# Kernel tuning notes

Hardware: AMD Instinct MI355X
Metric: run time of the kernel (lower is better)

## Reference

```python
import jax, jax.numpy as jnp
import numpy as np

DIM = 512
NUM_HEADS = 8
DIM_HEAD = DIM // NUM_HEADS


def _xavier(key, shape):
    fan_in, fan_out = shape[0], shape[1]
    a = (6.0 / (fan_in + fan_out)) ** 0.5
    return jax.random.uniform(key, shape, jnp.float32, -a, a)


def setup_inputs() -> dict:
    key = jax.random.key(0)
    ks = jax.random.split(key, 8)
    B, N, M = 2, 2048, 2048
    x = jax.random.normal(ks[0], (B, N, DIM), jnp.float32)
    source = jax.random.normal(ks[1], (B, M, DIM), jnp.float32)
    source_mask = jax.random.randint(ks[2], (B, M), 0, 2) > 0
    Wq = _xavier(ks[3], (DIM, DIM)); bq = jnp.zeros((DIM,), jnp.float32)
    Wk = _xavier(ks[4], (DIM, DIM)); bk = jnp.zeros((DIM,), jnp.float32)
    Wv = _xavier(ks[5], (DIM, DIM)); bv = jnp.zeros((DIM,), jnp.float32)
    Wm = _xavier(ks[6], (DIM, DIM)); bm = jnp.zeros((DIM,), jnp.float32)
    return {"x": x, "source": source, "source_mask": source_mask,
            "Wq": Wq, "bq": bq, "Wk": Wk, "bk": bk,
            "Wv": Wv, "bv": bv, "Wm": Wm, "bm": bm}


def reference(x, source, source_mask, Wq, bq, Wk, bk, Wv, bv, Wm, bm):
    B, N, D = x.shape
    M = source.shape[-2]
    H, Dh = NUM_HEADS, DIM_HEAD
    # projections (torch Linear: x @ W^T + b)
    q = (x @ Wq.T + bq).reshape(B, N, H, Dh)
    k = (source @ Wk.T + bk).reshape(B, M, H, Dh)
    v = (source @ Wv.T + bv).reshape(B, M, H, Dh)
    scale = 1.0 / (Dh ** 0.5)
    # scores: [B, N, M, H]
    scores = jnp.einsum('bnhd,bmhd->bnmh', q, k) * scale
    scores = jnp.where(source_mask[:, None, :, None], scores, -jnp.inf)
    prob = jax.nn.softmax(scores, axis=-2)  # softmax over m
    agg = jnp.einsum('bnmh,bmhd->bnhd', prob, v).reshape(B, N, D)
    return agg @ Wm.T + bm
```

## Files before the change

### kernel.cpp

```cpp
#include <hip/hip_runtime.h>
#include <hip/hip_bf16.h>

#define DIMF 512
#define NHEAD 8
#define DHEAD 64
#define BATCH 2
#define SEQN 2048
#define SEQM 2048
#define FPS 40
#define QSCALE 0.18033688011112042f

typedef unsigned short u16;
typedef __attribute__((ext_vector_type(8))) short bf16x8;
typedef __attribute__((ext_vector_type(4))) float f32x4;

static __device__ __forceinline__ u16 f2bf(float f) {
    unsigned u = __float_as_uint(f);
    u += 0x7FFF + ((u >> 16) & 1);
    return (u16)(u >> 16);
}
static __device__ __forceinline__ u16 f2bf_fast(float f) {
    return (u16)((__float_as_uint(f) + 0x8000u) >> 16);
}
static __device__ __forceinline__ ushort4 cvt4(float4 v) {
    return make_ushort4(f2bf(v.x), f2bf(v.y), f2bf(v.z), f2bf(v.w));
}
static __device__ __forceinline__ bf16x8 mask8(const int* p) {
    int4 a = *(const int4*)p;
    int4 b = *(const int4*)(p + 4);
    union { u16 u[8]; bf16x8 v; } r;
    r.u[0] = a.x ? 0x3F80 : 0; r.u[1] = a.y ? 0x3F80 : 0;
    r.u[2] = a.z ? 0x3F80 : 0; r.u[3] = a.w ? 0x3F80 : 0;
    r.u[4] = b.x ? 0x3F80 : 0; r.u[5] = b.y ? 0x3F80 : 0;
    r.u[6] = b.z ? 0x3F80 : 0; r.u[7] = b.w ? 0x3F80 : 0;
    return r.v;
}

static __device__ __forceinline__
void load16(const u16* g, u16* l) {
    __builtin_amdgcn_global_load_lds(
        (const __attribute__((address_space(1))) void*)g,
        (__attribute__((address_space(3))) void*)l,
        16, 0, 0);
}

#define ASZ (64 * FPS)
#define BSZ (128 * FPS)

__device__ __forceinline__
void gemm_mfma(const float* __restrict__ Xf, const u16* __restrict__ Xb,
               const float* __restrict__ Wf, const float* __restrict__ bias,
               const int* __restrict__ msk, void* __restrict__ Out, int mode)
{
    __shared__ __align__(16) u16 SH[2 * ASZ + 2 * BSZ];

    const int tid  = threadIdx.x;
    const int wave = tid >> 6;
    const int lane = tid & 63;
    const int l15  = lane & 15;
    const int quad = lane >> 4;
    const int wm = wave & 1, wn = wave >> 1;
    const int r0 = blockIdx.x * 64, c0 = blockIdx.y * 128;

    f32x4 acc[2][4] = {};

    const int wr = tid >> 1, wh = (tid & 1) * 16;
    const int ar = tid >> 3, aseg = tid & 7;
    const int br = tid >> 2, boct = tid & 3;

    float4 rw[4];
    float4 ra0, ra1;
    bf16x8 rab;

    auto loadg = [&](int k0) {
        #pragma unroll
        for (int j = 0; j < 4; ++j)
            rw[j] = *(const float4*)&Wf[(size_t)(c0 + wr) * DIMF + k0 + wh + 4 * j];
        if (Xf) {
            ra0 = *(const float4*)&Xf[(size_t)(r0 + ar) * DIMF + k0 + aseg * 4];
            ra1 = *(const float4*)&Xf[(size_t)(r0 + ar + 32) * DIMF + k0 + aseg * 4];
        } else {
            rab = *(const bf16x8*)&Xb[(size_t)(r0 + br) * DIMF + k0 + boct * 8];
        }
    };
    auto stage = [&](int buf) {
        u16* As = SH + buf * ASZ;
        u16* Bs = SH + 2 * ASZ + buf * BSZ;
        if (Xf) {
            *(ushort4*)&As[ar * FPS + aseg * 4] = cvt4(ra0);
            *(ushort4*)&As[(ar + 32) * FPS + aseg * 4] = cvt4(ra1);
        } else {
            *(bf16x8*)&As[br * FPS + boct * 8] = rab;
        }
        #pragma unroll
        for (int j = 0; j < 4; ++j)
            *(ushort4*)&Bs[wr * FPS + wh + 4 * j] = cvt4(rw[j]);
    };

    loadg(0);
    stage(0);
    loadg(32);
    __syncthreads();

    const int NK = DIMF / 32;
    for (int kt = 0; kt < NK; ++kt) {
        const int cur = kt & 1;
        if (kt + 1 < NK) stage(cur ^ 1);
        if (kt + 2 < NK) loadg((kt + 2) * 32);
        const u16* As = SH + cur * ASZ;
        const u16* Bs = SH + 2 * ASZ + cur * BSZ;

        bf16x8 af[2], bf[4];
        #pragma unroll
        for (int mi = 0; mi < 2; ++mi)
            af[mi] = *(const bf16x8*)&As[(wm * 32 + mi * 16 + l15) * FPS + quad * 8];
        #pragma unroll
        for (int ni = 0; ni < 4; ++ni)
            bf[ni] = *(const bf16x8*)&Bs[(wn * 64 + ni * 16 + l15) * FPS + quad * 8];
        #pragma unroll
        for (int mi = 0; mi < 2; ++mi)
            #pragma unroll
            for (int ni = 0; ni < 4; ++ni)
                acc[mi][ni] = __builtin_amdgcn_mfma_f32_16x16x32_bf16(
                    af[mi], bf[ni], acc[mi][ni], 0, 0, 0);
        __syncthreads();
    }

    float bb[4];
    #pragma unroll
    for (int ni = 0; ni < 4; ++ni)
        bb[ni] = bias[c0 + wn * 64 + ni * 16 + l15];

    if (mode == 2) {
        u16* T = SH;
        const int b = r0 >> 11;
        const int n_base = r0 & (SEQN - 1);
        #pragma unroll
        for (int hh = 0; hh < 2; ++hh) {
            __syncthreads();
            if (wn == hh) {
                #pragma unroll
                for (int mi = 0; mi < 2; ++mi) {
                    const int rl = wm * 32 + mi * 16 + quad * 4;
                    int4 m4 = *(const int4*)&msk[b * SEQM + n_base + rl];
                    float mm[4];
                    mm[0] = m4.x ? 1.f : 0.f; mm[1] = m4.y ? 1.f : 0.f;
                    mm[2] = m4.z ? 1.f : 0.f; mm[3] = m4.w ? 1.f : 0.f;
                    #pragma unroll
                    for (int ni = 0; ni < 4; ++ni)
                        #pragma unroll
                        for (int r = 0; r < 4; ++r)
                            T[(rl + r) * 72 + ni * 16 + l15] =
                                f2bf((acc[mi][ni][r] + bb[ni]) * mm[r]);
                }
            }
            __syncthreads();
            const int d = tid >> 2, ms = (tid & 3) << 4;
            u16 tmp[16];
            #pragma unroll
            for (int j = 0; j < 16; ++j) tmp[j] = T[(ms + j) * 72 + d];
            const int hgl = (c0 >> 6) + hh;
            u16* dst = (u16*)Out + ((size_t)(b * NHEAD + hgl) * DHEAD + d) * SEQM
                       + n_base + ms;
            *(bf16x8*)&dst[0] = *(bf16x8*)&tmp[0];
            *(bf16x8*)&dst[8] = *(bf16x8*)&tmp[8];
        }
        return;
    }

    #pragma unroll
    for (int mi = 0; mi < 2; ++mi) {
        const int Rbase = r0 + wm * 32 + mi * 16 + quad * 4;
        const int b = Rbase >> 11;
        const int nb = Rbase & (SEQN - 1);
        #pragma unroll
        for (int ni = 0; ni < 4; ++ni) {
            const int C = c0 + wn * 64 + ni * 16 + l15;
            const int h = C >> 6, d = C & 63;
            if (mode == 0) {
                u16* ow = (u16*)Out;
                #pragma unroll
                for (int r = 0; r < 4; ++r)
                    ow[(((size_t)(b * NHEAD + h) * SEQN) + nb + r) * DHEAD + d] =
                        f2bf((acc[mi][ni][r] + bb[ni]) * QSCALE);
            } else if (mode == 1) {
                u16* ow = (u16*)Out;
                #pragma unroll
                for (int r = 0; r < 4; ++r)
                    ow[(((size_t)(b * NHEAD + h) * SEQN) + nb + r) * DHEAD + d] =
                        f2bf(acc[mi][ni][r] + bb[ni]);
            } else {
                float* ow = (float*)Out;
                #pragma unroll
                for (int r = 0; r < 4; ++r)
                    ow[(size_t)(Rbase + r) * DIMF + C] = acc[mi][ni][r] + bb[ni];
            }
        }
    }
}

__global__ __launch_bounds__(256, 3)
void qkv_proj(const float* __restrict__ x, const float* __restrict__ src,
              const float* __restrict__ Wq, const float* __restrict__ bq,
              const float* __restrict__ Wk, const float* __restrict__ bk,
              const float* __restrict__ Wv, const float* __restrict__ bv,
              const int* __restrict__ mask,
              u16* __restrict__ qw, u16* __restrict__ kw, u16* __restrict__ vtw)
{
    const int z = blockIdx.z;
    const float* X = (z == 0) ? x : src;
    const float* W = (z == 0) ? Wq : (z == 1) ? Wk : Wv;
    const float* B = (z == 0) ? bq : (z == 1) ? bk : bv;
    void* O = (z == 0) ? (void*)qw : (z == 1) ? (void*)kw : (void*)vtw;
    gemm_mfma(X, nullptr, W, B, mask, O, z);
}

__global__ __launch_bounds__(256, 3)
void out_proj(const u16* __restrict__ aggb, const float* __restrict__ Wm,
              const float* __restrict__ bm, float* __restrict__ out)
{
    gemm_mfma(nullptr, aggb, Wm, bm, nullptr, (void*)out, 3);
}

__global__ __launch_bounds__(256, 4)
void flash_attn_mfma(const u16* __restrict__ q, const u16* __restrict__ k,
                     const u16* __restrict__ vt, const int* __restrict__ mask,
                     u16* __restrict__ agg)
{
    __shared__ __align__(16) u16 KsD[2][4096];
    __shared__ __align__(16) u16 VtsD[2][4096];
    __shared__ u16 Ps[4 * 16 * FPS];
    float* Osum = (float*)&KsD[0][0];
    float* Lsum = (float*)&VtsD[0][0];

    const int tid  = threadIdx.x;
    const int wave = tid >> 6;
    const int lane = tid & 63;
    const int l15  = lane & 15;
    const int quad = lane >> 4;
    const int qg = wave >> 1, mh = wave & 1;

    const int bid  = blockIdx.x;
    const int xcd  = bid & 7, slot = bid >> 3;
    const int pair = (xcd << 1) | (slot & 1);
    const int b = pair >> 3, h = pair & 7;
    const int n0 = (slot >> 1) * 32;

    const size_t hoff = (size_t)(b * NHEAD + h) * (size_t)SEQM * DHEAD;
    const u16* kb = k  + hoff;
    const u16* vb = vt + hoff;
    const int* mg = mask + b * SEQM;

    const int dr   = lane >> 3;
    const int doct = (lane & 7) ^ (dr & 7);
    const int g0 = wave, g1 = 4 + wave;
    const u16* kq0 = kb + (size_t)(g0 * 8 + dr) * DHEAD + doct * 8;
    const u16* kq1 = kb + (size_t)(g1 * 8 + dr) * DHEAD + doct * 8;
    const u16* vq0 = vb + (size_t)(g0 * 8 + dr) * SEQM + doct * 8;
    const u16* vq1 = vb + (size_t)(g1 * 8 + dr) * SEQM + doct * 8;

    bf16x8 qf[2];
    {
        const u16* qp = q + hoff + (size_t)(n0 + qg * 16 + l15) * DHEAD + quad * 8;
        qf[0] = *(const bf16x8*)qp;
        qf[1] = *(const bf16x8*)(qp + 32);
    }

    load16(kq0, &KsD[0][g0 * 512]);
    load16(kq1, &KsD[0][g1 * 512]);
    load16(vq0, &VtsD[0][g0 * 512]);
    load16(vq1, &VtsD[0][g1 * 512]);
    bf16x8 mf_nxt = mask8(&mg[32 * mh + quad * 8]);

    f32x4 O[4] = {};
    f32x4 lacc = {};
    u16* Pw = Ps + wave * (16 * FPS);
    const int xoct = l15 & 7;

    for (int mt = 0; mt < SEQM / 64; ++mt) {
        const int cur = mt & 1;
        __syncthreads();
        bf16x8 mf = mf_nxt;
        if (mt + 1 < SEQM / 64) {
            const int m1 = (mt + 1) * 64;
            const int nb = cur ^ 1;
            load16(kq0 + (size_t)m1 * DHEAD, &KsD[nb][g0 * 512]);
            load16(kq1 + (size_t)m1 * DHEAD, &KsD[nb][g1 * 512]);
            load16(vq0 + m1, &VtsD[nb][g0 * 512]);
            load16(vq1 + m1, &VtsD[nb][g1 * 512]);
            mf_nxt = mask8(&mg[m1 + 32 * mh + quad * 8]);
        }
        const u16* Ks  = KsD[cur];
        const u16* Vts = VtsD[cur];

        f32x4 st[2] = {};
        #pragma unroll
        for (int sub = 0; sub < 2; ++sub) {
            const int mrow = 32 * mh + 16 * sub + l15;
            #pragma unroll
            for (int c = 0; c < 2; ++c) {
                const int oct = (4 * c + quad) ^ xoct;
                bf16x8 af = *(const bf16x8*)&Ks[mrow * 64 + oct * 8];
                st[sub] = __builtin_amdgcn_mfma_f32_16x16x32_bf16(
                    af, qf[c], st[sub], 0, 0, 0);
            }
        }

        #pragma unroll
        for (int sub = 0; sub < 2; ++sub) {
            ushort4 w4 = make_ushort4(
                f2bf_fast(__builtin_amdgcn_exp2f(st[sub][0])),
                f2bf_fast(__builtin_amdgcn_exp2f(st[sub][1])),
                f2bf_fast(__builtin_amdgcn_exp2f(st[sub][2])),
                f2bf_fast(__builtin_amdgcn_exp2f(st[sub][3])));
            *(ushort4*)&Pw[l15 * FPS + 16 * sub + 4 * quad] = w4;
        }

        bf16x8 pf = *(const bf16x8*)&Pw[l15 * FPS + quad * 8];
        lacc = __builtin_amdgcn_mfma_f32_16x16x32_bf16(pf, mf, lacc, 0, 0, 0);
        #pragma unroll
        for (int sd = 0; sd < 4; ++sd) {
            const int oct = (4 * mh + quad) ^ xoct;
            bf16x8 vf = *(const bf16x8*)&Vts[(16 * sd + l15) * 64 + oct * 8];
            O[sd] = __builtin_amdgcn_mfma_f32_16x16x32_bf16(pf, vf, O[sd], 0, 0, 0);
        }
    }

    __syncthreads();
    if (mh == 1) {
        #pragma unroll
        for (int sd = 0; sd < 4; ++sd)
            #pragma unroll
            for (int r = 0; r < 4; ++r)
                Osum[qg * 1024 + (quad * 4 + r) * 64 + 16 * sd + l15] = O[sd][r];
        if (l15 == 0) {
            #pragma unroll
            for (int r = 0; r < 4; ++r) Lsum[qg * 16 + quad * 4 + r] = lacc[r];
        }
    }
    __syncthreads();
    if (mh == 0) {
        #pragma unroll
        for (int r = 0; r < 4; ++r) {
            const float inv = 1.f / (lacc[r] + Lsum[qg * 16 + quad * 4 + r]);
            const int n = n0 + qg * 16 + quad * 4 + r;
            u16* ag = agg + ((size_t)b * SEQN + n) * DIMF + h * DHEAD + l15;
            #pragma unroll
            for (int sd = 0; sd < 4; ++sd)
                ag[16 * sd] = f2bf((O[sd][r] +
                    Osum[qg * 1024 + (quad * 4 + r) * 64 + 16 * sd + l15]) * inv);
        }
    }
}

extern "C" void kernel_launch(void* const* d_in, const int* in_sizes, int n_in,
                              void* d_out, int out_size, void* d_ws, size_t ws_size,
                              hipStream_t stream)
{
    (void)in_sizes; (void)n_in; (void)out_size; (void)ws_size;
    const float* x      = (const float*)d_in[0];
    const float* source = (const float*)d_in[1];
    const int*   mask   = (const int*)  d_in[2];
    const float* Wq = (const float*)d_in[3]; const float* bq = (const float*)d_in[4];
    const float* Wk = (const float*)d_in[5]; const float* bk = (const float*)d_in[6];
    const float* Wv = (const float*)d_in[7]; const float* bv = (const float*)d_in[8];
    const float* Wm = (const float*)d_in[9]; const float* bm = (const float*)d_in[10];
    float* out = (float*)d_out;

    const size_t SZ = (size_t)BATCH * SEQN * DIMF;
    u16* qw   = (u16*)d_ws;
    u16* kw   = qw  + SZ;
    u16* vtw  = kw  + SZ;
    u16* aggb = vtw + SZ;

    dim3 gproj(4096 / 64, 512 / 128, 3);
    qkv_proj<<<gproj, 256, 0, stream>>>(x, source, Wq, bq, Wk, bk, Wv, bv,
                                        mask, qw, kw, vtw);

    flash_attn_mfma<<<1024, 256, 0, stream>>>(qw, kw, vtw, mask, aggb);

    dim3 gout(4096 / 64, 512 / 128);
    out_proj<<<gout, 256, 0, stream>>>(aggb, Wm, bm, out);
}
```

Measured before the change: 158.8 us.

## Double query rows per attention block to reuse K/V tiles across two query groups

Each flash-attention block now handles 64 query rows instead of 32, with every wave computing two 16-row query subtiles that share the same K and V fragments loaded from LDS. This halves the grid to 512 blocks and halves total K/V global and LDS traffic per query. In exchange it uses more registers (occupancy hint lowered to 3), a larger P scratch buffer and a larger Osum reduction region, and gives fewer blocks for the 256 CUs.

```diff
diff --git a/kernel.cpp b/kernel.cpp
--- a/kernel.cpp
+++ b/kernel.cpp
@@ -222,14 +222,14 @@
     gemm_mfma(nullptr, aggb, Wm, bm, nullptr, (void*)out, 3);
 }
 
-__global__ __launch_bounds__(256, 4)
+__global__ __launch_bounds__(256, 3)
 void flash_attn_mfma(const u16* __restrict__ q, const u16* __restrict__ k,
                      const u16* __restrict__ vt, const int* __restrict__ mask,
                      u16* __restrict__ agg)
 {
     __shared__ __align__(16) u16 KsD[2][4096];
     __shared__ __align__(16) u16 VtsD[2][4096];
-    __shared__ u16 Ps[4 * 16 * FPS];
+    __shared__ u16 Ps[4 * 32 * FPS];
     float* Osum = (float*)&KsD[0][0];
     float* Lsum = (float*)&VtsD[0][0];
 
@@ -244,7 +244,7 @@
     const int xcd  = bid & 7, slot = bid >> 3;
     const int pair = (xcd << 1) | (slot & 1);
     const int b = pair >> 3, h = pair & 7;
-    const int n0 = (slot >> 1) * 32;
+    const int n0 = (slot >> 1) * 64;
 
     const size_t hoff = (size_t)(b * NHEAD + h) * (size_t)SEQM * DHEAD;
     const u16* kb = k  + hoff;
@@ -259,11 +259,13 @@
     const u16* vq0 = vb + (size_t)(g0 * 8 + dr) * SEQM + doct * 8;
     const u16* vq1 = vb + (size_t)(g1 * 8 + dr) * SEQM + doct * 8;
 
-    bf16x8 qf[2];
-    {
-        const u16* qp = q + hoff + (size_t)(n0 + qg * 16 + l15) * DHEAD + quad * 8;
-        qf[0] = *(const bf16x8*)qp;
-        qf[1] = *(const bf16x8*)(qp + 32);
+    bf16x8 qf[2][2];
+    #pragma unroll
+    for (int qh = 0; qh < 2; ++qh) {
+        const u16* qp = q + hoff + (size_t)(n0 + qg * 32 + qh * 16 + l15) * DHEAD
+                        + quad * 8;
+        qf[qh][0] = *(const bf16x8*)qp;
+        qf[qh][1] = *(const bf16x8*)(qp + 32);
     }
 
     load16(kq0, &KsD[0][g0 * 512]);
@@ -272,9 +274,9 @@
     load16(vq1, &VtsD[0][g1 * 512]);
     bf16x8 mf_nxt = mask8(&mg[32 * mh + quad * 8]);
 
-    f32x4 O[4] = {};
-    f32x4 lacc = {};
-    u16* Pw = Ps + wave * (16 * FPS);
+    f32x4 O[2][4] = {};
+    f32x4 lacc[2] = {};
+    u16* Pw = Ps + wave * (32 * FPS);
     const int xoct = l15 & 7;
 
     for (int mt = 0; mt < SEQM / 64; ++mt) {
@@ -293,7 +295,7 @@
         const u16* Ks  = KsD[cur];
         const u16* Vts = VtsD[cur];
 
-        f32x4 st[2] = {};
+        f32x4 st[2][2] = {};
         #pragma unroll
         for (int sub = 0; sub < 2; ++sub) {
             const int mrow = 32 * mh + 16 * sub + l15;
@@ -301,55 +303,76 @@
             for (int c = 0; c < 2; ++c) {
                 const int oct = (4 * c + quad) ^ xoct;
                 bf16x8 af = *(const bf16x8*)&Ks[mrow * 64 + oct * 8];
-                st[sub] = __builtin_amdgcn_mfma_f32_16x16x32_bf16(
-                    af, qf[c], st[sub], 0, 0, 0);
-            }
-        }
-
-        #pragma unroll
-        for (int sub = 0; sub < 2; ++sub) {
-            ushort4 w4 = make_ushort4(
-                f2bf_fast(__builtin_amdgcn_exp2f(st[sub][0])),
-                f2bf_fast(__builtin_amdgcn_exp2f(st[sub][1])),
-                f2bf_fast(__builtin_amdgcn_exp2f(st[sub][2])),
-                f2bf_fast(__builtin_amdgcn_exp2f(st[sub][3])));
-            *(ushort4*)&Pw[l15 * FPS + 16 * sub + 4 * quad] = w4;
-        }
-
-        bf16x8 pf = *(const bf16x8*)&Pw[l15 * FPS + quad * 8];
-        lacc = __builtin_amdgcn_mfma_f32_16x16x32_bf16(pf, mf, lacc, 0, 0, 0);
+                #pragma unroll
+                for (int qh = 0; qh < 2; ++qh)
+                    st[qh][sub] = __builtin_amdgcn_mfma_f32_16x16x32_bf16(
+                        af, qf[qh][c], st[qh][sub], 0, 0, 0);
+            }
+        }
+
+        #pragma unroll
+        for (int qh = 0; qh < 2; ++qh)
+            #pragma unroll
+            for (int sub = 0; sub < 2; ++sub) {
+                ushort4 w4 = make_ushort4(
+                    f2bf_fast(__builtin_amdgcn_exp2f(st[qh][sub][0])),
+                    f2bf_fast(__builtin_amdgcn_exp2f(st[qh][sub][1])),
+                    f2bf_fast(__builtin_amdgcn_exp2f(st[qh][sub][2])),
+                    f2bf_fast(__builtin_amdgcn_exp2f(st[qh][sub][3])));
+                *(ushort4*)&Pw[(qh * 16 + l15) * FPS + 16 * sub + 4 * quad] = w4;
+            }
+
+        bf16x8 vf[4];
         #pragma unroll
         for (int sd = 0; sd < 4; ++sd) {
             const int oct = (4 * mh + quad) ^ xoct;
-            bf16x8 vf = *(const bf16x8*)&Vts[(16 * sd + l15) * 64 + oct * 8];
-            O[sd] = __builtin_amdgcn_mfma_f32_16x16x32_bf16(pf, vf, O[sd], 0, 0, 0);
+            vf[sd] = *(const bf16x8*)&Vts[(16 * sd + l15) * 64 + oct * 8];
+        }
+
+        #pragma unroll
+        for (int qh = 0; qh < 2; ++qh) {
+            bf16x8 pf = *(const bf16x8*)&Pw[(qh * 16 + l15) * FPS + quad * 8];
+            lacc[qh] = __builtin_amdgcn_mfma_f32_16x16x32_bf16(pf, mf, lacc[qh], 0, 0, 0);
+            #pragma unroll
+            for (int sd = 0; sd < 4; ++sd)
+                O[qh][sd] = __builtin_amdgcn_mfma_f32_16x16x32_bf16(
+                    pf, vf[sd], O[qh][sd], 0, 0, 0);
         }
     }
 
     __syncthreads();
     if (mh == 1) {
         #pragma unroll
-        for (int sd = 0; sd < 4; ++sd)
-            #pragma unroll
-            for (int r = 0; r < 4; ++r)
-                Osum[qg * 1024 + (quad * 4 + r) * 64 + 16 * sd + l15] = O[sd][r];
-        if (l15 == 0) {
-            #pragma unroll
-            for (int r = 0; r < 4; ++r) Lsum[qg * 16 + quad * 4 + r] = lacc[r];
+        for (int qh = 0; qh < 2; ++qh) {
+            #pragma unroll
+            for (int sd = 0; sd < 4; ++sd)
+                #pragma unroll
+                for (int r = 0; r < 4; ++r)
+                    Osum[qg * 2048 + (qh * 16 + quad * 4 + r) * 64 + 16 * sd + l15]
+                        = O[qh][sd][r];
+            if (l15 == 0) {
+                #pragma unroll
+                for (int r = 0; r < 4; ++r)
+                    Lsum[qg * 32 + qh * 16 + quad * 4 + r] = lacc[qh][r];
+            }
         }
     }
     __syncthreads();
     if (mh == 0) {
         #pragma unroll
-        for (int r = 0; r < 4; ++r) {
-            const float inv = 1.f / (lacc[r] + Lsum[qg * 16 + quad * 4 + r]);
-            const int n = n0 + qg * 16 + quad * 4 + r;
-            u16* ag = agg + ((size_t)b * SEQN + n) * DIMF + h * DHEAD + l15;
-            #pragma unroll
-            for (int sd = 0; sd < 4; ++sd)
-                ag[16 * sd] = f2bf((O[sd][r] +
-                    Osum[qg * 1024 + (quad * 4 + r) * 64 + 16 * sd + l15]) * inv);
-        }
+        for (int qh = 0; qh < 2; ++qh)
+            #pragma unroll
+            for (int r = 0; r < 4; ++r) {
+                const float inv = 1.f /
+                    (lacc[qh][r] + Lsum[qg * 32 + qh * 16 + quad * 4 + r]);
+                const int n = n0 + qg * 32 + qh * 16 + quad * 4 + r;
+                u16* ag = agg + ((size_t)b * SEQN + n) * DIMF + h * DHEAD + l15;
+                #pragma unroll
+                for (int sd = 0; sd < 4; ++sd)
+                    ag[16 * sd] = f2bf((O[qh][sd][r] +
+                        Osum[qg * 2048 + (qh * 16 + quad * 4 + r) * 64 + 16 * sd + l15])
+                        * inv);
+            }
     }
 }
 
@@ -377,7 +400,7 @@
     qkv_proj<<<gproj, 256, 0, stream>>>(x, source, Wq, bq, Wk, bk, Wv, bv,
                                         mask, qw, kw, vtw);
 
-    flash_attn_mfma<<<1024, 256, 0, stream>>>(qw, kw, vtw, mask, aggb);
+    flash_attn_mfma<<<512, 256, 0, stream>>>(qw, kw, vtw, mask, aggb);
 
     dim3 gout(4096 / 64, 512 / 128);
     out_proj<<<gout, 256, 0, stream>>>(aggb, Wm, bm, out);
```

New measurement: 156.0 us. No clear change (-1.8%).
